# Optimization experiments

Hardware: AMD Instinct MI355X
Metric: run time of the kernel (lower is better)

## Reference

```python
import math
import jax, jax.numpy as jnp
import numpy as np

B, CIN, COUT, K, S = 2, 64, 64, 3, 18  # batch, channels, kernel size per dim, spatial size per dim


def setup_inputs() -> dict:
    key = jax.random.key(0)
    k1, k2 = jax.random.split(key)
    inputs = jax.random.normal(k1, (B, CIN, S, S, S, S), dtype=jnp.float32)
    std = 1.0 / math.sqrt(CIN * K ** 4)  # matches init_weight: 1/sqrt(in_channels * n_offsets)
    kernel = jax.random.uniform(k2, (K ** 4, CIN, COUT), dtype=jnp.float32, minval=-std, maxval=std)
    return {"inputs": inputs, "kernel": kernel}


def reference(inputs, kernel):
    # kernel: [k0*k1*k2*k3, Cin, Cout], offsets enumerated row-major over the 4 kernel dims.
    # Equivalent to the per-offset matmul + shift-accumulate in conv4d (valid padding,
    # stride=1, dilation=1), expressed as a single 4-spatial-dim XLA convolution.
    cin, cout = kernel.shape[1], kernel.shape[2]
    w = kernel.reshape(K, K, K, K, cin, cout).transpose(5, 4, 0, 1, 2, 3)  # OIWXYZ
    out = jax.lax.conv_general_dilated(
        inputs, w,
        window_strides=(1, 1, 1, 1),
        padding='VALID',
        rhs_dilation=(1, 1, 1, 1),
        dimension_numbers=('NCWXYZ', 'OIWXYZ', 'NCWXYZ'),
    )  # [B, Cout, 16, 16, 16, 16]
    return out
```

## Files before the change

kernel.cpp:

```cpp
#include <hip/hip_runtime.h>


typedef __attribute__((ext_vector_type(8))) short bf16x8;
typedef __attribute__((ext_vector_type(4))) float f32x4;
typedef __attribute__((ext_vector_type(8))) unsigned short ushort8;
typedef unsigned short u16;
typedef unsigned int u32;

#define S_OFF_BYTES 663552u
#define WS_NEEDED   27537408u

__device__ __forceinline__ u16 f2bf(float f) {
    u32 u = __float_as_uint(f);
    u += 0x7FFFu + ((u >> 16) & 1u);
    return (u16)(u >> 16);
}

__global__ __launch_bounds__(256) void wprep(const float* __restrict__ ker, u16* __restrict__ wg) {
    const int g = blockIdx.x * 256 + threadIdx.x;
    const int l = g & 63, ks = (g >> 6) & 1, rt = (g >> 7) & 3, off = g >> 9;
    const int co  = rt * 16 + (l & 15);
    const int ci0 = ks * 32 + (l >> 4) * 8;
    const float* p = ker + (size_t)off * 4096 + co;
    ushort8 v;
#pragma unroll
    for (int e = 0; e < 8; ++e) v[e] = f2bf(p[(size_t)(ci0 + e) * 64]);
    *(ushort8*)(wg + (size_t)g * 8) = v;
}

__global__ __launch_bounds__(256) void sprep(const float* __restrict__ in, u16* __restrict__ s) {
    __shared__ u16 L[64 * 330];
    const int blk = blockIdx.x;
    const int b = blk / 324, wx = blk - b * 324;
    const float* src = in + (size_t)b * 6718464 + (wx / 18) * 5832 + (wx % 18) * 324;
    const int t = threadIdx.x;
    for (int i = t; i < 5184; i += 256) {
        const int ci = i / 81, j = i - ci * 81;
        float4 v = *(const float4*)(src + (size_t)ci * 104976 + j * 4);
        u32* q = (u32*)&L[ci * 330 + j * 4];
        q[0] = f2bf(v.x) | ((u32)f2bf(v.y) << 16);
        q[1] = f2bf(v.z) | ((u32)f2bf(v.w) << 16);
    }
    __syncthreads();
    u16* dst = s + (size_t)blk * 20736;
    for (int i = t; i < 2592; i += 256) {
        const int ks = i / 1296, r4 = i - ks * 1296;
        const int rem = r4 >> 2, g = r4 & 3;
        ushort8 v;
#pragma unroll
        for (int e = 0; e < 8; ++e) v[e] = L[(ks * 32 + g * 8 + e) * 330 + rem];
        const int gp = g ^ ((rem >> 1) & 3);
        *(ushort8*)(dst + ks * 10368 + rem * 32 + gp * 8) = v;
    }
}

__global__ __launch_bounds__(256, 2)
void conv4d_main(const u16* __restrict__ wg, const u16* __restrict__ s, float* __restrict__ out) {
    __shared__ u16 A[3][6144];
    __shared__ u16 Bq[2][10368];

    const int bid = blockIdx.x;
    const int bs  = (bid & 7) * 64 + (bid >> 3);
    const int b   = bs >> 8;
    const int w   = (bs >> 4) & 15;
    const int x   = bs & 15;

    const int t  = threadIdx.x, wv = t >> 6, l = t & 63;
    const int lg = l >> 4, ll = l & 15;

    f32x4 acc[4][4];
#pragma unroll
    for (int i = 0; i < 4; ++i)
#pragma unroll
        for (int j = 0; j < 4; ++j) acc[i][j] = (f32x4){0.f, 0.f, 0.f, 0.f};

    const u16* sb = s + (size_t)(b * 324 + w * 18 + x) * 20736;

    bf16x8 af[2][3][4];
    bf16x8 bb[2][6];

#define STAGE_A(tk, KZ)                                                                  \
    do {                                                                                 \
        const int kwx_ = (tk) >> 1, ks2_ = (tk) & 1;                                     \
        _Pragma("unroll")                                                                \
        for (int c_ = 0; c_ < 3; ++c_) {                                                 \
            const u16* src_ = wg + (size_t)(kwx_ * 9 + c_ * 3 + (KZ)) * 4096             \
                              + wv * 1024 + ks2_ * 512 + l * 8;                          \
            __builtin_amdgcn_global_load_lds(                                            \
                (const __attribute__((address_space(1))) u32*)src_,                      \
                (__attribute__((address_space(3))) u32*)&A[KZ][c_ * 2048 + wv * 512 + l * 8], \
                16, 0, 0);                                                               \
        }                                                                                \
    } while (0)

#define STAGE_B(h)                                                                       \
    do {                                                                                 \
        const int kwx_ = (h) >> 1, ks_ = (h) & 1;                                        \
        const int kw_ = kwx_ / 3, kx_ = kwx_ - kw_ * 3;                                  \
        const u16* src_ = sb + (size_t)(kw_ * 18 + kx_) * 20736 + ks_ * 10368;           \
        const int base_ = wv * 324;                                                      \
        _Pragma("unroll")                                                                \
        for (int k_ = 0; k_ < 5; ++k_) {                                                 \
            const int i_ = base_ + k_ * 64 + l;                                          \
            __builtin_amdgcn_global_load_lds(                                            \
                (const __attribute__((address_space(1))) u32*)(src_ + (size_t)i_ * 8),   \
                (__attribute__((address_space(3))) u32*)&Bq[(h) & 1][i_ * 8], 16, 0, 0); \
        }                                                                                \
        if (l < 4) {                                                                     \
            const int i_ = base_ + 320 + l;                                              \
            __builtin_amdgcn_global_load_lds(                                            \
                (const __attribute__((address_space(1))) u32*)(src_ + (size_t)i_ * 8),   \
                (__attribute__((address_space(3))) u32*)&Bq[(h) & 1][i_ * 8], 16, 0, 0); \
        }                                                                                \
    } while (0)

#define READ_REGS(BK, UP, QQ)                                                            \
    do {                                                                                 \
        const int tk_ = (UP) / 3;                                                        \
        const u16* Tb_ = Bq[tk_ & 1];                                                    \
        _Pragma("unroll")                                                                \
        for (int ky_ = 0; ky_ < 3; ++ky_)                                                \
            _Pragma("unroll")                                                            \
            for (int rt_ = 0; rt_ < 4; ++rt_)                                            \
                af[BK][ky_][rt_] = *(const bf16x8*)&A[QQ][ky_ * 2048 + rt_ * 512 + l * 8]; \
        _Pragma("unroll")                                                                \
        for (int j_ = 0; j_ < 6; ++j_) {                                                 \
            const int rem_ = (4 * wv + j_) * 18 + ll + (QQ);                             \
            bb[BK][j_] = *(const bf16x8*)&Tb_[rem_ * 32 + ((lg ^ ((rem_ >> 1) & 3)) << 3)]; \
        }                                                                                \
    } while (0)

#define MFMA_PHASE(BK)                                                                   \
    do {                                                                                 \
        __builtin_amdgcn_s_setprio(1);                                                   \
        _Pragma("unroll")                                                                \
        for (int ky_ = 0; ky_ < 3; ++ky_)                                                \
            _Pragma("unroll")                                                            \
            for (int ct_ = 0; ct_ < 4; ++ct_)                                            \
                _Pragma("unroll")                                                        \
                for (int rt_ = 0; rt_ < 4; ++rt_)                                        \
                    acc[rt_][ct_] = __builtin_amdgcn_mfma_f32_16x16x32_bf16(             \
                        af[BK][ky_][rt_], bb[BK][ct_ + ky_], acc[rt_][ct_], 0, 0, 0);    \
        __builtin_amdgcn_s_setprio(0);                                                   \
    } while (0)

    STAGE_A(0, 0);
    STAGE_A(0, 1);
    STAGE_B(0);
    asm volatile("s_waitcnt vmcnt(0)" ::: "memory");
    __builtin_amdgcn_sched_barrier(0);
    __builtin_amdgcn_s_barrier();
    READ_REGS(0, 0, 0);

    for (int u6 = 0; u6 < 54; u6 += 6) {
#pragma unroll
        for (int m = 0; m < 6; ++m) {
            const int u = u6 + m;
            if (u < 52) STAGE_A((u + 2) / 3, ((m + 2) % 3));
            if ((m % 3) == 1) {
                const int p_ = u / 3;
                if (p_ < 17) STAGE_B(p_ + 1);
            }
            if (u < 53) READ_REGS(((m + 1) & 1), (u + 1), ((m + 1) % 3));
            __builtin_amdgcn_sched_barrier(0);
            MFMA_PHASE((m & 1));
            if (u < 53) {
                asm volatile("s_waitcnt vmcnt(0)" ::: "memory");
                __builtin_amdgcn_sched_barrier(0);
                __builtin_amdgcn_s_barrier();
            }
        }
    }
#undef STAGE_A
#undef STAGE_B
#undef READ_REGS
#undef MFMA_PHASE

    float* ob = out + (size_t)b * 4194304 + (size_t)w * 4096 + (size_t)x * 256;
#pragma unroll
    for (int rt = 0; rt < 4; ++rt) {
        const int co0 = rt * 16 + 4 * lg;
#pragma unroll
        for (int ct = 0; ct < 4; ++ct) {
            const int base = (4 * wv + ct) * 16 + ll;
#pragma unroll
            for (int r = 0; r < 4; ++r)
                ob[(size_t)(co0 + r) * 65536 + base] = acc[rt][ct][r];
        }
    }
}

__global__ __launch_bounds__(512, 2)
void conv4d_mfma(const float* __restrict__ in, const float* __restrict__ ker,
                 float* __restrict__ out) {
    __shared__ unsigned short T[18 * 18 * 64];
    __shared__ unsigned short Wt[2][64 * 64];
    const int bx = blockIdx.x;
    const int b = bx >> 8, wsp = (bx >> 4) & 15, x = bx & 15;
    const int t = threadIdx.x, wv = t >> 6, l = t & 63;
    const int lg = l >> 4, ll = l & 15;
    const float* inb = in + (size_t)b * 6718464 + wsp * 5832 + x * 324;
    f32x4 acc[4][2];
#pragma unroll
    for (int i = 0; i < 4; ++i)
#pragma unroll
        for (int j = 0; j < 2; ++j) acc[i][j] = (f32x4){0.f, 0.f, 0.f, 0.f};
#pragma unroll
    for (int f0 = 0; f0 < 4096; f0 += 512) {
        const int f = f0 + t, ci = f >> 6, co = f & 63;
        Wt[0][co * 64 + ((((ci >> 3) ^ (co & 7)) << 3) | (ci & 7))] = f2bf(ker[f]);
    }
    for (int off = 0; off < 81; ++off) {
        const int sub = off % 9;
        if (sub == 0) {
            const int kw = off / 27, kx = (off / 9) % 3;
            const float* p = inb + kw * 5832 + kx * 324;
            for (int f = t; f < 18 * 18 * 64; f += 512) {
                const int ci = f / 324, rem = f - ci * 324, zp = rem % 18;
                T[rem * 64 + ((((ci >> 3) ^ (zp & 7)) << 3) | (ci & 7))] =
                    f2bf(p[(size_t)ci * 104976 + rem]);
            }
        }
        if (off + 1 < 81) {
            const float* p = ker + (off + 1) * 4096;
            unsigned short* wb = Wt[(off + 1) & 1];
#pragma unroll
            for (int f0 = 0; f0 < 4096; f0 += 512) {
                const int f = f0 + t, ci = f >> 6, co = f & 63;
                wb[co * 64 + ((((ci >> 3) ^ (co & 7)) << 3) | (ci & 7))] = f2bf(p[f]);
            }
        }
        if (sub == 0) __syncthreads();
        const int ky = sub / 3, kz = sub - ky * 3;
        const int zp = ll + kz, zs = zp & 7;
#pragma unroll
        for (int ks = 0; ks < 2; ++ks) {
            bf16x8 af[4];
#pragma unroll
            for (int rt = 0; rt < 4; ++rt)
                af[rt] = *(const bf16x8*)&Wt[off & 1][(rt * 16 + ll) * 64 + (((lg + 4 * ks) ^ (ll & 7)) << 3)];
#pragma unroll
            for (int ct = 0; ct < 2; ++ct) {
                const int rem = (2 * wv + ct + ky) * 18 + zp;
                const bf16x8 bfr = *(const bf16x8*)&T[rem * 64 + (((lg + 4 * ks) ^ zs) << 3)];
#pragma unroll
                for (int rt = 0; rt < 4; ++rt)
                    acc[rt][ct] = __builtin_amdgcn_mfma_f32_16x16x32_bf16(af[rt], bfr, acc[rt][ct], 0, 0, 0);
            }
        }
        __syncthreads();
    }
    float* ob = out + (size_t)b * 4194304 + wsp * 4096 + x * 256;
#pragma unroll
    for (int rt = 0; rt < 4; ++rt) {
        const int co0 = rt * 16 + 4 * lg;
#pragma unroll
        for (int ct = 0; ct < 2; ++ct) {
            const int base = (2 * wv + ct) * 16 + ll;
#pragma unroll
            for (int r = 0; r < 4; ++r)
                ob[(size_t)(co0 + r) * 65536 + base] = acc[rt][ct][r];
        }
    }
}

extern "C" void kernel_launch(void* const* d_in, const int* in_sizes, int n_in,
                              void* d_out, int out_size, void* d_ws, size_t ws_size,
                              hipStream_t stream) {
    const float* in  = (const float*)d_in[0];
    const float* ker = (const float*)d_in[1];
    float* out = (float*)d_out;
    if (ws_size >= (size_t)WS_NEEDED) {
        u16* wg = (u16*)d_ws;
        u16* s  = (u16*)((char*)d_ws + S_OFF_BYTES);
        wprep<<<dim3(162), dim3(256), 0, stream>>>(ker, wg);
        sprep<<<dim3(648), dim3(256), 0, stream>>>(in, s);
        conv4d_main<<<dim3(512), dim3(256), 0, stream>>>(wg, s, out);
    } else {
        conv4d_mfma<<<dim3(512), dim3(512), 0, stream>>>(in, ker, out);
    }
}
```

Before: 93.53 us.

## Read A fragments per-ky in-phase and relax vmcnt waits to overlap loads

Instead of prefetching all three ky slices of A into registers a stage early, A fragments are now read from LDS just in time, interleaved with the MFMA groups. This shrinks the A register buffer. The vmcnt waits are changed from 0 to partial counts so that some in-flight global-to-LDS loads stay outstanding across barriers. B staging is moved earlier, and launch bounds are dropped to one block per SM, presumably to free registers. The risks are more LDS-read latency exposed inside the MFMA stream, lower occupancy, and correctness hazards if the partial wait counts do not match the issued loads.

```diff
diff --git a/kernel.cpp b/kernel.cpp
--- a/kernel.cpp
+++ b/kernel.cpp
@@ -54,7 +54,7 @@
     }
 }
 
-__global__ __launch_bounds__(256, 2)
+__global__ __launch_bounds__(256, 1)
 void conv4d_main(const u16* __restrict__ wg, const u16* __restrict__ s, float* __restrict__ out) {
     __shared__ u16 A[3][6144];
     __shared__ u16 Bq[2][10368];
@@ -76,7 +76,7 @@
 
     const u16* sb = s + (size_t)(b * 324 + w * 18 + x) * 20736;
 
-    bf16x8 af[2][3][4];
+    bf16x8 af[2][4];
     bf16x8 bb[2][6];
 
 #define STAGE_A(tk, KZ)                                                                  \
@@ -114,15 +114,16 @@
         }                                                                                \
     } while (0)
 
-#define READ_REGS(BK, UP, QQ)                                                            \
-    do {                                                                                 \
-        const int tk_ = (UP) / 3;                                                        \
-        const u16* Tb_ = Bq[tk_ & 1];                                                    \
-        _Pragma("unroll")                                                                \
-        for (int ky_ = 0; ky_ < 3; ++ky_)                                                \
-            _Pragma("unroll")                                                            \
-            for (int rt_ = 0; rt_ < 4; ++rt_)                                            \
-                af[BK][ky_][rt_] = *(const bf16x8*)&A[QQ][ky_ * 2048 + rt_ * 512 + l * 8]; \
+#define READ_A(BK, SLOT, KY)                                                             \
+    do {                                                                                 \
+        _Pragma("unroll")                                                                \
+        for (int rt_ = 0; rt_ < 4; ++rt_)                                                \
+            af[BK][rt_] = *(const bf16x8*)&A[SLOT][(KY) * 2048 + rt_ * 512 + l * 8];     \
+    } while (0)
+
+#define READ_B(BK, TKPAR, QQ)                                                            \
+    do {                                                                                 \
+        const u16* Tb_ = Bq[TKPAR];                                                      \
         _Pragma("unroll")                                                                \
         for (int j_ = 0; j_ < 6; ++j_) {                                                 \
             const int rem_ = (4 * wv + j_) * 18 + ll + (QQ);                             \
@@ -130,51 +131,60 @@
         }                                                                                \
     } while (0)
 
-#define MFMA_PHASE(BK)                                                                   \
+#define MFMA16(ABK, BBK, KY)                                                             \
     do {                                                                                 \
         __builtin_amdgcn_s_setprio(1);                                                   \
         _Pragma("unroll")                                                                \
-        for (int ky_ = 0; ky_ < 3; ++ky_)                                                \
+        for (int ct_ = 0; ct_ < 4; ++ct_)                                                \
             _Pragma("unroll")                                                            \
-            for (int ct_ = 0; ct_ < 4; ++ct_)                                            \
-                _Pragma("unroll")                                                        \
-                for (int rt_ = 0; rt_ < 4; ++rt_)                                        \
-                    acc[rt_][ct_] = __builtin_amdgcn_mfma_f32_16x16x32_bf16(             \
-                        af[BK][ky_][rt_], bb[BK][ct_ + ky_], acc[rt_][ct_], 0, 0, 0);    \
+            for (int rt_ = 0; rt_ < 4; ++rt_)                                            \
+                acc[rt_][ct_] = __builtin_amdgcn_mfma_f32_16x16x32_bf16(                 \
+                    af[ABK][rt_], bb[BBK][ct_ + (KY)], acc[rt_][ct_], 0, 0, 0);          \
         __builtin_amdgcn_s_setprio(0);                                                   \
+    } while (0)
+
+#define WAITBAR(N)                                                                       \
+    do {                                                                                 \
+        asm volatile("s_waitcnt vmcnt(" #N ")" ::: "memory");                            \
+        __builtin_amdgcn_sched_barrier(0);                                               \
+        __builtin_amdgcn_s_barrier();                                                    \
     } while (0)
 
     STAGE_A(0, 0);
     STAGE_A(0, 1);
     STAGE_B(0);
-    asm volatile("s_waitcnt vmcnt(0)" ::: "memory");
-    __builtin_amdgcn_sched_barrier(0);
-    __builtin_amdgcn_s_barrier();
-    READ_REGS(0, 0, 0);
+    WAITBAR(0);
+    READ_B(0, 0, 0);
 
     for (int u6 = 0; u6 < 54; u6 += 6) {
 #pragma unroll
         for (int m = 0; m < 6; ++m) {
             const int u = u6 + m;
-            if (u < 52) STAGE_A((u + 2) / 3, ((m + 2) % 3));
-            if ((m % 3) == 1) {
-                const int p_ = u / 3;
-                if (p_ < 17) STAGE_B(p_ + 1);
-            }
-            if (u < 53) READ_REGS(((m + 1) & 1), (u + 1), ((m + 1) % 3));
+            const int cb = m & 1;
+            if (u < 52) STAGE_A((u + 2) / 3, (m + 2) % 3);
+            if (m % 3 == 0 && u < 51) STAGE_B(u / 3 + 1);
+            READ_A(0, m % 3, 0);
+            if (u < 53) READ_B(cb ^ 1, (((m + 1) / 3) & 1), (m + 1) % 3);
+            READ_A(1, m % 3, 1);
             __builtin_amdgcn_sched_barrier(0);
-            MFMA_PHASE((m & 1));
+            MFMA16(0, cb, 0);
+            READ_A(0, m % 3, 2);
+            __builtin_amdgcn_sched_barrier(0);
+            MFMA16(1, cb, 1);
+            __builtin_amdgcn_sched_barrier(0);
+            MFMA16(0, cb, 2);
             if (u < 53) {
-                asm volatile("s_waitcnt vmcnt(0)" ::: "memory");
-                __builtin_amdgcn_sched_barrier(0);
-                __builtin_amdgcn_s_barrier();
+                if (m % 3 == 0) { if (u < 51) WAITBAR(9); else WAITBAR(3); }
+                else            { if (u < 52) WAITBAR(3); else WAITBAR(0); }
             }
         }
     }
 #undef STAGE_A
 #undef STAGE_B
-#undef READ_REGS
-#undef MFMA_PHASE
+#undef READ_A
+#undef READ_B
+#undef MFMA16
+#undef WAITBAR
 
     float* ob = out + (size_t)b * 4194304 + (size_t)w * 4096 + (size_t)x * 256;
 #pragma unroll
```

Measured after the change: 92.18 us. No clear change (-1.4%).

## Use two-wave blocks with larger per-wave tiles and direct global weight loads

Applied to the files above, without the earlier changes.

Shrinks conv4d_main blocks from four waves to two, and each wave now covers eight column tiles instead of four, which doubles the accumulators. Weight fragments are read straight from global memory (L2-cached) into registers instead of being staged through LDS, so the A shared buffers and their barriers go away and the input tile is synchronised only once per three kz steps. The goal is more reuse of each weight fragment per wave and less LDS traffic and barrier cost. In exchange, register pressure rises sharply (128 accumulator floats plus fragments), occupancy falls to one block per launch-bound, and weight loads may expose global-memory latency.

```diff
diff --git a/kernel.cpp b/kernel.cpp
--- a/kernel.cpp
+++ b/kernel.cpp
@@ -54,10 +54,9 @@
     }
 }
 
-__global__ __launch_bounds__(256, 2)
+__global__ __launch_bounds__(128, 1)
 void conv4d_main(const u16* __restrict__ wg, const u16* __restrict__ s, float* __restrict__ out) {
-    __shared__ u16 A[3][6144];
-    __shared__ u16 Bq[2][10368];
+    __shared__ u16 Bs[2][10368];
 
     const int bid = blockIdx.x;
     const int bs  = (bid & 7) * 64 + (bid >> 3);
@@ -68,75 +67,68 @@
     const int t  = threadIdx.x, wv = t >> 6, l = t & 63;
     const int lg = l >> 4, ll = l & 15;
 
-    f32x4 acc[4][4];
+    f32x4 acc[4][8];
 #pragma unroll
     for (int i = 0; i < 4; ++i)
 #pragma unroll
-        for (int j = 0; j < 4; ++j) acc[i][j] = (f32x4){0.f, 0.f, 0.f, 0.f};
+        for (int j = 0; j < 8; ++j) acc[i][j] = (f32x4){0.f, 0.f, 0.f, 0.f};
 
     const u16* sb = s + (size_t)(b * 324 + w * 18 + x) * 20736;
 
     bf16x8 af[2][3][4];
-    bf16x8 bb[2][6];
-
-#define STAGE_A(tk, KZ)                                                                  \
-    do {                                                                                 \
-        const int kwx_ = (tk) >> 1, ks2_ = (tk) & 1;                                     \
-        _Pragma("unroll")                                                                \
-        for (int c_ = 0; c_ < 3; ++c_) {                                                 \
-            const u16* src_ = wg + (size_t)(kwx_ * 9 + c_ * 3 + (KZ)) * 4096             \
-                              + wv * 1024 + ks2_ * 512 + l * 8;                          \
-            __builtin_amdgcn_global_load_lds(                                            \
-                (const __attribute__((address_space(1))) u32*)src_,                      \
-                (__attribute__((address_space(3))) u32*)&A[KZ][c_ * 2048 + wv * 512 + l * 8], \
-                16, 0, 0);                                                               \
-        }                                                                                \
-    } while (0)
+    bf16x8 bb[2][10];
 
 #define STAGE_B(h)                                                                       \
     do {                                                                                 \
         const int kwx_ = (h) >> 1, ks_ = (h) & 1;                                        \
         const int kw_ = kwx_ / 3, kx_ = kwx_ - kw_ * 3;                                  \
         const u16* src_ = sb + (size_t)(kw_ * 18 + kx_) * 20736 + ks_ * 10368;           \
-        const int base_ = wv * 324;                                                      \
-        _Pragma("unroll")                                                                \
-        for (int k_ = 0; k_ < 5; ++k_) {                                                 \
+        const int base_ = wv * 648;                                                      \
+        _Pragma("unroll")                                                                \
+        for (int k_ = 0; k_ < 10; ++k_) {                                                \
             const int i_ = base_ + k_ * 64 + l;                                          \
             __builtin_amdgcn_global_load_lds(                                            \
                 (const __attribute__((address_space(1))) u32*)(src_ + (size_t)i_ * 8),   \
-                (__attribute__((address_space(3))) u32*)&Bq[(h) & 1][i_ * 8], 16, 0, 0); \
+                (__attribute__((address_space(3))) u32*)&Bs[(h) & 1][i_ * 8], 16, 0, 0); \
         }                                                                                \
-        if (l < 4) {                                                                     \
-            const int i_ = base_ + 320 + l;                                              \
+        if (l < 8) {                                                                     \
+            const int i_ = base_ + 640 + l;                                              \
             __builtin_amdgcn_global_load_lds(                                            \
                 (const __attribute__((address_space(1))) u32*)(src_ + (size_t)i_ * 8),   \
-                (__attribute__((address_space(3))) u32*)&Bq[(h) & 1][i_ * 8], 16, 0, 0); \
+                (__attribute__((address_space(3))) u32*)&Bs[(h) & 1][i_ * 8], 16, 0, 0); \
         }                                                                                \
     } while (0)
 
-#define READ_REGS(BK, UP, QQ)                                                            \
-    do {                                                                                 \
-        const int tk_ = (UP) / 3;                                                        \
-        const u16* Tb_ = Bq[tk_ & 1];                                                    \
+#define LOAD_AF(BK, U)                                                                   \
+    do {                                                                                 \
+        const int tk_ = (U) / 3, kz_ = (U) % 3;                                          \
+        const int kwx_ = tk_ >> 1, ks_ = tk_ & 1;                                        \
         _Pragma("unroll")                                                                \
         for (int ky_ = 0; ky_ < 3; ++ky_)                                                \
             _Pragma("unroll")                                                            \
             for (int rt_ = 0; rt_ < 4; ++rt_)                                            \
-                af[BK][ky_][rt_] = *(const bf16x8*)&A[QQ][ky_ * 2048 + rt_ * 512 + l * 8]; \
-        _Pragma("unroll")                                                                \
-        for (int j_ = 0; j_ < 6; ++j_) {                                                 \
-            const int rem_ = (4 * wv + j_) * 18 + ll + (QQ);                             \
+                af[BK][ky_][rt_] = *(const bf16x8*)(wg                                   \
+                    + (size_t)(kwx_ * 9 + ky_ * 3 + kz_) * 4096                          \
+                    + (size_t)(rt_ * 2 + ks_) * 512 + l * 8);                            \
+    } while (0)
+
+#define READ_BB(BK, P, KZ)                                                               \
+    do {                                                                                 \
+        const u16* Tb_ = Bs[(P) & 1];                                                    \
+        _Pragma("unroll")                                                                \
+        for (int j_ = 0; j_ < 10; ++j_) {                                                \
+            const int rem_ = (8 * wv + j_) * 18 + ll + (KZ);                             \
             bb[BK][j_] = *(const bf16x8*)&Tb_[rem_ * 32 + ((lg ^ ((rem_ >> 1) & 3)) << 3)]; \
         }                                                                                \
     } while (0)
 
-#define MFMA_PHASE(BK)                                                                   \
+#define MFMA96(BK)                                                                       \
     do {                                                                                 \
         __builtin_amdgcn_s_setprio(1);                                                   \
         _Pragma("unroll")                                                                \
         for (int ky_ = 0; ky_ < 3; ++ky_)                                                \
             _Pragma("unroll")                                                            \
-            for (int ct_ = 0; ct_ < 4; ++ct_)                                            \
+            for (int ct_ = 0; ct_ < 8; ++ct_)                                            \
                 _Pragma("unroll")                                                        \
                 for (int rt_ = 0; rt_ < 4; ++rt_)                                        \
                     acc[rt_][ct_] = __builtin_amdgcn_mfma_f32_16x16x32_bf16(             \
@@ -144,45 +136,43 @@
         __builtin_amdgcn_s_setprio(0);                                                   \
     } while (0)
 
-    STAGE_A(0, 0);
-    STAGE_A(0, 1);
     STAGE_B(0);
+    LOAD_AF(0, 0);
     asm volatile("s_waitcnt vmcnt(0)" ::: "memory");
     __builtin_amdgcn_sched_barrier(0);
     __builtin_amdgcn_s_barrier();
-    READ_REGS(0, 0, 0);
 
     for (int u6 = 0; u6 < 54; u6 += 6) {
 #pragma unroll
         for (int m = 0; m < 6; ++m) {
             const int u = u6 + m;
-            if (u < 52) STAGE_A((u + 2) / 3, ((m + 2) % 3));
-            if ((m % 3) == 1) {
-                const int p_ = u / 3;
-                if (p_ < 17) STAGE_B(p_ + 1);
-            }
-            if (u < 53) READ_REGS(((m + 1) & 1), (u + 1), ((m + 1) % 3));
-            __builtin_amdgcn_sched_barrier(0);
-            MFMA_PHASE((m & 1));
-            if (u < 53) {
+            const int p = u / 3;
+            const int q = m % 3;
+            const int cur = m & 1, nxt = cur ^ 1;
+            if (q == 0) READ_BB(cur, p, 0);
+            if (q == 0 && p + 1 < 18) STAGE_B(p + 1);
+            if (u + 1 < 54) LOAD_AF(nxt, u + 1);
+            if (q < 2) READ_BB(nxt, p, q + 1);
+            MFMA96(cur);
+            if (q == 2 && u < 53) {
                 asm volatile("s_waitcnt vmcnt(0)" ::: "memory");
                 __builtin_amdgcn_sched_barrier(0);
                 __builtin_amdgcn_s_barrier();
             }
         }
     }
-#undef STAGE_A
 #undef STAGE_B
-#undef READ_REGS
-#undef MFMA_PHASE
+#undef LOAD_AF
+#undef READ_BB
+#undef MFMA96
 
     float* ob = out + (size_t)b * 4194304 + (size_t)w * 4096 + (size_t)x * 256;
 #pragma unroll
     for (int rt = 0; rt < 4; ++rt) {
         const int co0 = rt * 16 + 4 * lg;
 #pragma unroll
-        for (int ct = 0; ct < 4; ++ct) {
-            const int base = (4 * wv + ct) * 16 + ll;
+        for (int ct = 0; ct < 8; ++ct) {
+            const int base = (8 * wv + ct) * 16 + ll;
 #pragma unroll
             for (int r = 0; r < 4; ++r)
                 ob[(size_t)(co0 + r) * 65536 + base] = acc[rt][ct][r];
@@ -275,7 +265,7 @@
         u16* s  = (u16*)((char*)d_ws + S_OFF_BYTES);
         wprep<<<dim3(162), dim3(256), 0, stream>>>(ker, wg);
         sprep<<<dim3(648), dim3(256), 0, stream>>>(in, s);
-        conv4d_main<<<dim3(512), dim3(256), 0, stream>>>(wg, s, out);
+        conv4d_main<<<dim3(512), dim3(128), 0, stream>>>(wg, s, out);
     } else {
         conv4d_mfma<<<dim3(512), dim3(512), 0, stream>>>(in, ker, out);
     }
```

Result: no change. 92.40 us (-1.2%).
